# Kernel tuning notes

Measured on AMD Instinct MI355X. Metric: run time of the kernel, lower is better.

The kernel has to match this reference:

```python
import jax, jax.numpy as jnp
import numpy as np
from jax import lax

D_MODEL = 1024
D_INNER = 2 * D_MODEL          # expand=2
D_STATE = 16
D_CONV = 4
DT_RANK = 64                   # ceil(1024/16)
DT_MIN = 0.001
DT_MAX = 0.1
BATCH = 4
SEQ = 2048


def setup_inputs() -> dict:
    key = jax.random.key(0)
    ks = jax.random.split(key, 8)
    s = lambda fan_in: 1.0 / np.sqrt(fan_in)
    x = jax.random.normal(ks[0], (BATCH, SEQ, D_MODEL), dtype=jnp.float32)
    # Linear weights stored as (in, out) so y = x @ W
    W_in = jax.random.uniform(ks[1], (D_MODEL, 2 * D_INNER), jnp.float32, -s(D_MODEL), s(D_MODEL))
    conv_w = jax.random.uniform(ks[2], (D_INNER, 1, D_CONV), jnp.float32, -s(D_CONV), s(D_CONV))
    conv_b = jax.random.uniform(ks[3], (D_INNER,), jnp.float32, -s(D_CONV), s(D_CONV))
    W_x = jax.random.uniform(ks[4], (D_INNER, DT_RANK + 2 * D_STATE), jnp.float32, -s(D_INNER), s(D_INNER))
    W_dt = jax.random.uniform(ks[5], (DT_RANK, D_INNER), jnp.float32, -s(DT_RANK), s(DT_RANK))
    b_dt = jax.random.uniform(ks[6], (D_INNER,), jnp.float32, -s(DT_RANK), s(DT_RANK))
    # A = arange(1..d_state) repeated over d_inner; store log(A)
    A_log = jnp.log(jnp.broadcast_to(jnp.arange(1, D_STATE + 1, dtype=jnp.float32), (D_INNER, D_STATE)))
    D_param = jnp.ones((D_INNER,), dtype=jnp.float32)
    W_out = jax.random.uniform(ks[7], (D_INNER, D_MODEL), jnp.float32, -s(D_INNER), s(D_INNER))
    return {"x": x, "W_in": W_in, "conv_w": conv_w, "conv_b": conv_b,
            "W_x": W_x, "W_dt": W_dt, "b_dt": b_dt, "A_log": A_log,
            "D_param": D_param, "W_out": W_out}


def reference(x, W_in, conv_w, conv_b, W_x, W_dt, b_dt, A_log, D_param, W_out):
    # in_proj + split
    xz = x @ W_in                                   # (B, S, 2*d_inner)
    x_branch, z_branch = jnp.split(xz, 2, axis=-1)  # each (B, S, d_inner)

    # causal depthwise conv1d (torch pads d_conv-1 both sides then slices [:seq])
    xc = jnp.pad(x_branch.transpose(0, 2, 1), ((0, 0), (0, 0), (D_CONV - 1, 0)))
    xc = lax.conv_general_dilated(xc, conv_w, (1,), 'VALID',
                                  dimension_numbers=('NCH', 'OIH', 'NCH'),
                                  feature_group_count=D_INNER)
    xc = xc + conv_b[None, :, None]
    x_conv = jax.nn.silu(xc.transpose(0, 2, 1))     # (B, S, d_inner)

    # input-dependent dt, B, C
    x_dbl = x_conv @ W_x                            # (B, S, dt_rank + 2*d_state)
    dt_low = x_dbl[..., :DT_RANK]
    Bm = x_dbl[..., DT_RANK:DT_RANK + D_STATE]      # (B, S, d_state)
    Cm = x_dbl[..., DT_RANK + D_STATE:]             # (B, S, d_state)
    dt = jax.nn.sigmoid(dt_low @ W_dt + b_dt) * (DT_MAX - DT_MIN) + DT_MIN
    dt = jnp.maximum(dt, 1e-4)                      # (B, S, d_inner)

    A = -jnp.exp(A_log)                             # (d_inner, d_state)

    # selective scan over time (n_substeps = 1)
    def step(h, inp):
        dt_t, B_t, C_t, x_t = inp                   # (B,di), (B,ds), (B,ds), (B,di)
        dA = jnp.exp(dt_t[:, :, None] * A[None])    # (B, di, ds)
        h = dA * h + (dt_t * x_t)[:, :, None] * B_t[:, None, :]
        y_t = jnp.sum(h * C_t[:, None, :], axis=-1) # (B, di)
        return h, y_t

    h0 = jnp.zeros((x.shape[0], D_INNER, D_STATE), dtype=x.dtype)
    _, ys = lax.scan(step, h0,
                     (dt.swapaxes(0, 1), Bm.swapaxes(0, 1),
                      Cm.swapaxes(0, 1), x_conv.swapaxes(0, 1)))
    y = ys.swapaxes(0, 1)                           # (B, S, d_inner)

    y = y + x_conv * D_param
    y = y * jax.nn.silu(z_branch)
    return y @ W_out                                # (B, S, d_model)
```

## Files before the change

kernel.cpp:

```cpp
#include <hip/hip_runtime.h>

typedef unsigned short u16;
typedef unsigned int u32;
typedef __attribute__((ext_vector_type(8))) short short8;
typedef __attribute__((ext_vector_type(4))) short short4v;
typedef __attribute__((ext_vector_type(2))) short short2v;
typedef __attribute__((ext_vector_type(4))) float f32x4;

#define NBATCH 4
#define NSEQ   2048
#define DMODEL 1024
#define DINNER 2048
#define DSTATE 16
#define DTRANK 64
#define ROWS   (NBATCH*NSEQ)
#define NCH    64
#define CLEN   32

__device__ __forceinline__ float b2f(u16 u){ union{u32 i; float f;} v; v.i=((u32)u)<<16; return v.f; }
__device__ __forceinline__ u16 f2b(float f){ union{float f; u32 i;} v; v.f=f; u32 i=v.i; return (u16)((i + 0x7FFFu + ((i>>16)&1u))>>16); }
__device__ __forceinline__ float sigmoidf_(float x){ return 1.0f/(1.0f+__expf(-x)); }

__global__ __launch_bounds__(256) void prep(const u16* __restrict__ x,
    const u16* __restrict__ Win, const u16* __restrict__ convw,
    const u16* __restrict__ Wx, const u16* __restrict__ Wdt,
    const u16* __restrict__ Alog, const u16* __restrict__ Wout,
    const u16* __restrict__ v0, const u16* __restrict__ v1, const u16* __restrict__ v2,
    int* __restrict__ meta){
  __shared__ int vote;
  __shared__ int mxbits;
  const int tid = threadIdx.x;
  const u16* V[3] = {v0, v1, v2};

  const u16* ptrs[6] = {x, Win, convw, Wx, Wdt, Wout};
  const float bounds[6] = {8.f, 0.045f, 0.6f, 0.035f, 0.15f, 0.035f};
  const int slots[6] = {0, 1, 2, 4, 5, 9};
  for (int q = 0; q < 6; q++){
    if (tid == 0) vote = 1;
    __syncthreads();
    int bad = 0;
    for (int i = tid; i < 2048; i += 256){
      float v = fabsf(b2f(ptrs[q][i]));
      if (!(v <= bounds[q])) bad = 1;
    }
    if (bad) atomicAnd(&vote, 0);
    __syncthreads();
    if (tid == 0) meta[slots[q]] = vote;
    __syncthreads();
  }
  if (tid == 0){ u16 u = Alog[1]; meta[7] = (u == 0x3F31 || u == 0x3F32) ? 1 : 0; }

  int iD = -1, fD = 1;
  for (int k = 0; k < 3; k++){
    if (V[k][0] == 0x3F80 && V[k][1] == 0x3F80){ iD = k; fD = 1; }
    else if (V[k][0] == 0 && V[k][1] == 0x3F80 && V[k][2] == 0){ iD = k; fD = 0; }
  }
  if (iD < 0){ iD = 2; fD = 1; }
  int oo[2], no = 0;
  for (int k = 0; k < 3; k++) if (k != iD) oo[no++] = k;
  int fo[2]; float mo[2];
  for (int q = 0; q < 2; q++){
    if (tid == 0) vote = 1;
    __syncthreads();
    int bad = 0;
    for (int i = tid; i < 2048; i += 256){
      float v = fabsf(b2f(V[oo[q]][i]));
      if (!(v <= 0.6f)) bad = 1;
    }
    if (bad) atomicAnd(&vote, 0);
    __syncthreads();
    fo[q] = vote;
    if (tid == 0) mxbits = 0;
    __syncthreads();
    float m = 0.f;
    for (int i = tid; i < 2048; i += 256){
      float v = fabsf(fo[q] ? b2f(V[oo[q]][i]) : ((const float*)V[oo[q]])[i]);
      m = fmaxf(m, v);
    }
    atomicMax(&mxbits, __float_as_int(m));
    __syncthreads();
    mo[q] = __int_as_float(mxbits);
    __syncthreads();
  }
  if (tid == 0){
    int a = (mo[0] > 0.25f) ? 0 : 1;
    meta[10] = oo[a];     meta[3] = fo[a];
    meta[11] = oo[1-a];   meta[6] = fo[1-a];
    meta[12] = iD;        meta[8] = fD;
  }
}

__global__ __launch_bounds__(256) void cvt_bf16(const void* __restrict__ in,
                                                u16* __restrict__ out, long n,
                                                const int* __restrict__ meta, int slot){
  long i = (long)blockIdx.x*256 + threadIdx.x;
  if (i >= n) return;
  if (meta[slot]) out[i] = ((const u16*)in)[i];
  else            out[i] = f2b(((const float*)in)[i]);
}

__global__ __launch_bounds__(256) void cvt_x8(const void* __restrict__ in,
                                              u16* __restrict__ out,
                                              const int* __restrict__ meta){
  long i8 = ((long)blockIdx.x*256 + threadIdx.x)*8;
  if (meta[0]){
    *(short8*)(out + i8) = *(const short8*)((const u16*)in + i8);
  } else {
    const float* f = (const float*)in + i8;
    f32x4 a = *(const f32x4*)f;
    f32x4 b = *(const f32x4*)(f+4);
    short8 o;
    #pragma unroll
    for (int j=0;j<4;j++){ ((u16*)&o)[j] = f2b(a[j]); ((u16*)&o)[4+j] = f2b(b[j]); }
    *(short8*)(out + i8) = o;
  }
}

__global__ __launch_bounds__(256) void cvt_trio(const void* __restrict__ v0,
                                                const void* __restrict__ v1,
                                                const void* __restrict__ v2,
                                                const int* __restrict__ meta,
                                                u16* __restrict__ cbc,
                                                u16* __restrict__ bdtc,
                                                u16* __restrict__ dpc){
  int i = blockIdx.x*256 + threadIdx.x;
  int which = i >> 11, d = i & 2047;
  const void* V[3] = {v0, v1, v2};
  int src, fl; u16* dst;
  if (which == 0){ src = meta[10]; fl = meta[3]; dst = cbc; }
  else if (which == 1){ src = meta[11]; fl = meta[6]; dst = bdtc; }
  else { src = meta[12]; fl = meta[8]; dst = dpc; }
  dst[d] = fl ? ((const u16*)V[src])[d] : f2b(((const float*)V[src])[d]);
}

__global__ __launch_bounds__(256) void transpose_pad(const void* __restrict__ inv,
                                                     u16* __restrict__ out,
                                                     int K, int N, int Nout,
                                                     const int* __restrict__ meta, int slot){
  __shared__ u16 t[32][33];
  const int f = meta[slot];
  const u16*   ib = (const u16*)inv;
  const float* iff = (const float*)inv;
  int k0 = blockIdx.x*32, n0 = blockIdx.y*32;
  int tx = threadIdx.x & 31, ty = threadIdx.x >> 5;
  #pragma unroll
  for (int i=0;i<32;i+=8){
    int k = k0+ty+i, n = n0+tx;
    u16 v = 0;
    if (k<K && n<N) v = f ? ib[(long)k*N+n] : f2b(iff[(long)k*N+n]);
    t[ty+i][tx] = v;
  }
  __syncthreads();
  #pragma unroll
  for (int i=0;i<32;i+=8){
    int n = n0+ty+i, k = k0+tx;
    if (n<Nout && k<K) out[(long)n*K+k] = t[tx][ty+i];
  }
}

template<int MODE>
__global__ __launch_bounds__(256) void gemm_bt(
    const u16* __restrict__ A, int lda,
    const u16* __restrict__ Bt, int K,
    u16* __restrict__ C0, u16* __restrict__ C1, int ldc,
    const u16* __restrict__ bias, float* __restrict__ Cf)
{
  __shared__ u16 sa[128*64];
  __shared__ u16 sb[128*64];
  const int tid = threadIdx.x;
  const int lane = tid & 63;
  const int wave = tid >> 6;
  const int wm = (wave >> 1) * 64;
  const int wn = (wave & 1) * 64;
  const int lane15 = lane & 15;
  const int quad = lane >> 4;
  const long rowBase = (long)blockIdx.y * 128;
  const long colBase = (long)blockIdx.x * 128;

  int kbeg = 0, kend = K;
  if (MODE == 4){
    const int span = K >> 2;
    kbeg = blockIdx.z * span;
    kend = kbeg + span;
    Cf += (long)blockIdx.z * (8192L*128);
  }

  f32x4 acc[4][4];
  #pragma unroll
  for (int i=0;i<4;i++)
    #pragma unroll
    for (int j=0;j<4;j++)
      #pragma unroll
      for (int r=0;r<4;r++) acc[i][j][r]=0.0f;

  const int e  = tid*8;
  const int r0 = e >> 6;
  const int c0 = e & 63;

  for (int kb=kbeg; kb<kend; kb+=64) {
    #pragma unroll
    for (int i=0;i<4;i++){
      const u16* ga = A + (rowBase + r0 + i*32)*lda + kb + c0;
      __builtin_amdgcn_global_load_lds((const __attribute__((address_space(1))) void*)ga,
                                       (__attribute__((address_space(3))) void*)&sa[e + i*2048],
                                       16, 0, 0);
    }
    #pragma unroll
    for (int i=0;i<4;i++){
      const u16* gb = Bt + (colBase + r0 + i*32)*(long)K + kb + c0;
      __builtin_amdgcn_global_load_lds((const __attribute__((address_space(1))) void*)gb,
                                       (__attribute__((address_space(3))) void*)&sb[e + i*2048],
                                       16, 0, 0);
    }
    __syncthreads();
    #pragma unroll
    for (int ko=0; ko<2; ko++){
      const int kk = ko*32 + quad*8;
      short8 af[4], bfr[4];
      #pragma unroll
      for (int i=0;i<4;i++) af[i]  = *(const short8*)&sa[(wm + i*16 + lane15)*64 + kk];
      #pragma unroll
      for (int j=0;j<4;j++) bfr[j] = *(const short8*)&sb[(wn + j*16 + lane15)*64 + kk];
      #pragma unroll
      for (int i=0;i<4;i++)
        #pragma unroll
        for (int j=0;j<4;j++)
          acc[i][j] = __builtin_amdgcn_mfma_f32_16x16x32_bf16(af[i], bfr[j], acc[i][j], 0, 0, 0);
    }
    __syncthreads();
  }

  #pragma unroll
  for (int i=0;i<4;i++){
    #pragma unroll
    for (int j=0;j<4;j++){
      long row = rowBase + wm + i*16 + quad*4;
      long col = colBase + wn + j*16 + lane15;
      #pragma unroll
      for (int r=0;r<4;r++){
        float v = acc[i][j][r];
        long rr = row + r;
        if (MODE == 0) {
          C0[rr*ldc + col] = f2b(v);
        } else if (MODE == 2) {
          float t  = sigmoidf_(v + b2f(bias[col]));
          float dv = fmaxf(t*0.099f + 0.001f, 1e-4f);
          C0[rr*ldc + col] = f2b(dv);
        } else if (MODE == 3 || MODE == 4) {
          Cf[rr*ldc + col] = v;
        }
      }
    }
  }
}

__global__ __launch_bounds__(256) void reduce_xdbl(const float* __restrict__ P,
                                                   u16* __restrict__ out){
  const long i4 = ((long)blockIdx.x*256 + threadIdx.x)*4;
  f32x4 a = *(const f32x4*)(P + i4);
  f32x4 b = *(const f32x4*)(P + 1048576 + i4);
  f32x4 c = *(const f32x4*)(P + 2097152 + i4);
  f32x4 d = *(const f32x4*)(P + 3145728 + i4);
  short4v o;
  #pragma unroll
  for (int j=0;j<4;j++) ((u16*)&o)[j] = f2b(a[j]+b[j]+c[j]+d[j]);
  *(short4v*)(out + i4) = o;
}

template<int IB, int JB>
__device__ __forceinline__ void mm16(f32x4 (&acc)[8][4],
                                     const short8 (&Av)[4][2], const short8 (&Bv)[2][2]){
  #pragma unroll
  for (int s=0;s<2;s++)
    #pragma unroll
    for (int i=0;i<4;i++)
      #pragma unroll
      for (int j=0;j<2;j++)
        acc[IB+i][JB+j] = __builtin_amdgcn_mfma_f32_16x16x32_bf16(Av[i][s], Bv[j][s], acc[IB+i][JB+j], 0, 0, 0);
}

__device__ __forceinline__ void lda4(short8 (&dst)[4][2], const u16* s, int base, int k0, int k1){
  #pragma unroll
  for (int i=0;i<4;i++){
    dst[i][0] = *(const short8*)&s[base + i*1024 + k0];
    dst[i][1] = *(const short8*)&s[base + i*1024 + k1];
  }
}
__device__ __forceinline__ void ldb2(short8 (&dst)[2][2], const u16* s, int base, int k0, int k1){
  #pragma unroll
  for (int j=0;j<2;j++){
    dst[j][0] = *(const short8*)&s[base + j*1024 + k0];
    dst[j][1] = *(const short8*)&s[base + j*1024 + k1];
  }
}

#define GB_SYNC_IN()  do{ asm volatile("s_barrier" ::: "memory"); \
                          asm volatile("s_waitcnt lgkmcnt(0)" ::: "memory"); \
                          __builtin_amdgcn_sched_barrier(0); \
                          __builtin_amdgcn_s_setprio(1); }while(0)
#define GB_SYNC_OUT() do{ __builtin_amdgcn_s_setprio(0); \
                          asm volatile("s_barrier" ::: "memory"); }while(0)
#define GB_SYNC_OUT_VM() do{ __builtin_amdgcn_s_setprio(0); \
                          asm volatile("s_waitcnt vmcnt(6)" ::: "memory"); \
                          asm volatile("s_barrier" ::: "memory"); }while(0)

template<int MODE>
__global__ __launch_bounds__(512, 2) void gemm256(
    const u16* __restrict__ A, int lda,
    const u16* __restrict__ Bt, int K,
    u16* __restrict__ C0, u16* __restrict__ C1, int ldc,
    float* __restrict__ Cf)
{
  __shared__ u16 sa[2*16384];
  __shared__ u16 sb[2*16384];
  const int tid  = threadIdx.x;
  const int lane = tid & 63;
  const int wm   = (tid >> 6) >> 2;
  const int wn   = (tid >> 6) & 3;
  const int lane15 = lane & 15;
  const int quad   = lane >> 4;

  const int nwg  = gridDim.x * gridDim.y;
  const int orig = blockIdx.y * gridDim.x + blockIdx.x;
  const int swz  = (orig & 7) * (nwg >> 3) + (orig >> 3);
  const int bx   = swz % gridDim.x;
  const int by   = swz / gridDim.x;
  const long rowBase = (long)by * 256;
  const long colBase = (long)bx * 256;

  const int xorv = (lane15 & 7) << 3;
  const int k0   = (quad*8) ^ xorv;
  const int k1   = (32 + quad*8) ^ xorv;
  const int aBase = (wm*128 + lane15) * 64;
  const int bBase = (wn*64  + lane15) * 64;

  const int scol = ((tid & 7) ^ ((tid >> 3) & 7)) << 3;
  const int arow = tid >> 3;
  const int bsub = ((tid >> 8) & 1)*64 + ((tid & 255) >> 3);
  const int bdst = (tid & 7) * 8;

  f32x4 acc[8][4];
  #pragma unroll
  for (int i=0;i<8;i++)
    #pragma unroll
    for (int j=0;j<4;j++)
      #pragma unroll
      for (int r=0;r<4;r++) acc[i][j][r]=0.0f;

  const int nt = K >> 6;

  auto stageA = [&](int buf, int rs, int kb){
    const u16* g = A + (rowBase + rs + arow)*(long)lda + kb + scol;
    __builtin_amdgcn_global_load_lds((const __attribute__((address_space(1))) void*)g,
        (__attribute__((address_space(3))) void*)&sa[buf*16384 + rs*64 + tid*8], 16, 0, 0);
  };
  auto stageB = [&](int buf, int cq, int part, int kb){
    const int row = part*128 + cq*32 + bsub;
    const u16* g = Bt + (colBase + row)*(long)K + kb + scol;
    __builtin_amdgcn_global_load_lds((const __attribute__((address_space(1))) void*)g,
        (__attribute__((address_space(3))) void*)&sb[buf*16384 + row*64 + bdst], 16, 0, 0);
  };
  auto stageAh = [&](int buf, int h, int kb){ stageA(buf, h*64, kb); stageA(buf, 128 + h*64, kb); };
  auto stageBc = [&](int buf, int cq, int kb){ stageB(buf, cq, 0, kb); stageB(buf, cq, 1, kb); };

  stageAh(0,0,0);  stageBc(0,0,0);  stageAh(0,1,0);  stageBc(0,1,0);
  stageAh(1,0,64); stageBc(1,0,64); stageAh(1,1,64);
  asm volatile("s_waitcnt vmcnt(6)" ::: "memory");
  asm volatile("s_barrier" ::: "memory");

  const u16* sA0 = &sa[0];      const u16* sB0 = &sb[0];
  const u16* sA1 = &sa[16384];  const u16* sB1 = &sb[16384];
  short8 a0[4][2], a1[4][2], b0[2][2], b1[2][2];

  for (int it = 0; it < (nt >> 1); ++it){
    const int kb = it << 7;

    lda4(a0, sA0, aBase, k0, k1);
    ldb2(b0, sB0, bBase, k0, k1);
    stageBc(1, 1, kb + 64);
    GB_SYNC_IN();  mm16<0,0>(acc, a0, b0);  GB_SYNC_OUT();
    lda4(a1, sA0, aBase + 4096, k0, k1);
    stageAh(0, 0, kb + 128);
    GB_SYNC_IN();  mm16<4,0>(acc, a1, b0);  GB_SYNC_OUT();
    ldb2(b1, sB0, bBase + 2048, k0, k1);
    stageBc(0, 0, kb + 128);
    GB_SYNC_IN();  mm16<0,2>(acc, a0, b1);  GB_SYNC_OUT();
    stageAh(0, 1, kb + 128);
    GB_SYNC_IN();  mm16<4,2>(acc, a1, b1);  GB_SYNC_OUT_VM();

    lda4(a0, sA1, aBase, k0, k1);
    ldb2(b0, sB1, bBase, k0, k1);
    stageBc(0, 1, kb + 128);
    GB_SYNC_IN();  mm16<0,0>(acc, a0, b0);  GB_SYNC_OUT();
    lda4(a1, sA1, aBase + 4096, k0, k1);
    stageAh(1, 0, kb + 192);
    GB_SYNC_IN();  mm16<4,0>(acc, a1, b0);  GB_SYNC_OUT();
    ldb2(b1, sB1, bBase + 2048, k0, k1);
    stageBc(1, 0, kb + 192);
    GB_SYNC_IN();  mm16<0,2>(acc, a0, b1);  GB_SYNC_OUT();
    stageAh(1, 1, kb + 192);
    GB_SYNC_IN();  mm16<4,2>(acc, a1, b1);  GB_SYNC_OUT_VM();
  }

  #pragma unroll
  for (int i=0;i<8;i++){
    const long row = rowBase + wm*128 + i*16 + quad*4;
    #pragma unroll
    for (int j=0;j<4;j++){
      const long col = colBase + wn*64 + j*16 + lane15;
      #pragma unroll
      for (int r=0;r<4;r++){
        const float v = acc[i][j][r];
        const long rr = row + r;
        if (MODE == 1){
          if (col < 2048) C0[rr*2048 + col] = f2b(v);
          else            C1[rr*2048 + (col-2048)] = f2b(v);
        } else {
          Cf[rr*ldc + col] = v;
        }
      }
    }
  }
}

__global__ __launch_bounds__(256) void conv_silu(const u16* __restrict__ xb,
                                                 const u16* __restrict__ w,
                                                 const u16* __restrict__ bias,
                                                 u16* __restrict__ xc){
  long idx8 = ((long)blockIdx.x*256 + threadIdx.x) * 8;
  int d = (int)(idx8 & (DINNER-1));
  int s = (int)((idx8 >> 11) & (NSEQ-1));
  int b = (int)(idx8 >> 22);

  short8 bv = *(const short8*)(bias + d);
  short8 wv0 = *(const short8*)(w + d*4);
  short8 wv1 = *(const short8*)(w + d*4 + 8);
  short8 wv2 = *(const short8*)(w + d*4 + 16);
  short8 wv3 = *(const short8*)(w + d*4 + 24);
  u16 wl[32];
  #pragma unroll
  for (int q=0;q<8;q++){ wl[q] = ((u16*)&wv0)[q]; wl[8+q] = ((u16*)&wv1)[q];
                         wl[16+q] = ((u16*)&wv2)[q]; wl[24+q] = ((u16*)&wv3)[q]; }

  float acc[8];
  #pragma unroll
  for (int l=0;l<8;l++) acc[l] = b2f(((u16*)&bv)[l]);

  #pragma unroll
  for (int j=0;j<4;j++){
    int t = s - 3 + j;
    if (t >= 0){
      short8 xv = *(const short8*)(xb + ((long)(b*NSEQ + t))*DINNER + d);
      #pragma unroll
      for (int l=0;l<8;l++)
        acc[l] += b2f(((u16*)&xv)[l]) * b2f(wl[l*4 + j]);
    }
  }
  short8 ov;
  #pragma unroll
  for (int l=0;l<8;l++){ float y = acc[l]*sigmoidf_(acc[l]); ((u16*)&ov)[l] = f2b(y); }
  *(short8*)(xc + idx8) = ov;
}

__global__ __launch_bounds__(256) void scan_pass1(const u16* __restrict__ dt,
                                                  const u16* __restrict__ xc,
                                                  const u16* __restrict__ xdbl,
                                                  const u16* __restrict__ Alog,
                                                  float* __restrict__ hend,
                                                  float* __restrict__ sumdt){
  const int tid = threadIdx.x;
  const int d0 = blockIdx.x*512 + tid*2;
  const int c = blockIdx.y;
  const int b = blockIdx.z;
  __shared__ float sB[CLEN][DSTATE];
  for (int i=tid; i<CLEN*DSTATE; i+=256){
    int t = i >> 4, s = i & 15;
    sB[t][s] = b2f(xdbl[((long)(b*NSEQ + c*CLEN + t))*128 + DTRANK + s]);
  }
  bool fast = true;
  #pragma unroll
  for (int j=0;j<2;j++)
    #pragma unroll
    for (int s=0;s<DSTATE;s++){
      float a = -__expf(b2f(Alog[(d0+j)*DSTATE + s]));
      fast = fast && (fabsf(a + (float)(s+1)) < 0.03f*(float)(s+1));
    }
  __syncthreads();

  float h[2][DSTATE];
  #pragma unroll
  for (int j=0;j<2;j++)
    #pragma unroll
    for (int s=0;s<DSTATE;s++) h[j][s] = 0.0f;
  float sd[2] = {0.f,0.f};
  long base = ((long)(b*NSEQ + c*CLEN))*DINNER + d0;
  short2v dt2 = *(const short2v*)(dt + base);
  short2v x2  = *(const short2v*)(xc + base);
  if (fast){
    for (int t=0;t<CLEN;t++){
      long nxt = base + (long)((t+1<CLEN)?(t+1):t)*DINNER;
      short2v dtn = *(const short2v*)(dt + nxt);
      short2v xn  = *(const short2v*)(xc + nxt);
      float B[DSTATE];
      *(f32x4*)&B[0]  = *(const f32x4*)&sB[t][0];
      *(f32x4*)&B[4]  = *(const f32x4*)&sB[t][4];
      *(f32x4*)&B[8]  = *(const f32x4*)&sB[t][8];
      *(f32x4*)&B[12] = *(const f32x4*)&sB[t][12];
      #pragma unroll
      for (int j=0;j<2;j++){
        float dtv = b2f(((u16*)&dt2)[j]);
        float xv  = b2f(((u16*)&x2)[j]);
        float u = dtv*xv;
        sd[j] += dtv;
        float e1 = __expf(-dtv);
        float p = e1;
        #pragma unroll
        for (int s=0;s<DSTATE;s++){
          h[j][s] = fmaf(p, h[j][s], u*B[s]);
          p *= e1;
        }
      }
      dt2 = dtn; x2 = xn;
    }
  } else {
    float Acf[2][DSTATE];
    #pragma unroll
    for (int j=0;j<2;j++)
      #pragma unroll
      for (int s=0;s<DSTATE;s++) Acf[j][s] = -__expf(b2f(Alog[(d0+j)*DSTATE + s]));
    for (int t=0;t<CLEN;t++){
      long nxt = base + (long)((t+1<CLEN)?(t+1):t)*DINNER;
      short2v dtn = *(const short2v*)(dt + nxt);
      short2v xn  = *(const short2v*)(xc + nxt);
      float B[DSTATE];
      *(f32x4*)&B[0]  = *(const f32x4*)&sB[t][0];
      *(f32x4*)&B[4]  = *(const f32x4*)&sB[t][4];
      *(f32x4*)&B[8]  = *(const f32x4*)&sB[t][8];
      *(f32x4*)&B[12] = *(const f32x4*)&sB[t][12];
      #pragma unroll
      for (int j=0;j<2;j++){
        float dtv = b2f(((u16*)&dt2)[j]);
        float xv  = b2f(((u16*)&x2)[j]);
        float u = dtv*xv;
        sd[j] += dtv;
        #pragma unroll
        for (int s=0;s<DSTATE;s++){
          float dA = __expf(dtv * Acf[j][s]);
          h[j][s] = fmaf(dA, h[j][s], u*B[s]);
        }
      }
      dt2 = dtn; x2 = xn;
    }
  }
  #pragma unroll
  for (int j=0;j<2;j++){
    long hidx = ((long)(b*DINNER + d0 + j)*NCH + c)*DSTATE;
    #pragma unroll
    for (int q=0;q<4;q++) *(f32x4*)&hend[hidx + q*4] = *(const f32x4*)&h[j][q*4];
    sumdt[(long)(b*DINNER + d0 + j)*NCH + c] = sd[j];
  }
}

__global__ __launch_bounds__(256) void scan_pass2(float* __restrict__ hend,
                                                  const float* __restrict__ sumdt,
                                                  const u16* __restrict__ Alog){
  long i = (long)blockIdx.x*256 + threadIdx.x;
  int s = (int)(i & 15);
  long bd = i >> 4;
  int d = (int)(bd & (DINNER-1));
  float A = -__expf(b2f(Alog[d*DSTATE + s]));
  float run = 0.0f;
  long base = bd*NCH*DSTATE + s;
  for (int c=0;c<NCH;c++){
    float e = hend[base + (long)c*DSTATE];
    float decay = __expf(A * sumdt[bd*NCH + c]);
    hend[base + (long)c*DSTATE] = run;
    run = run*decay + e;
  }
}

__global__ __launch_bounds__(256) void scan_pass3(const u16* __restrict__ dt,
                                                  u16* __restrict__ xc,
                                                  const u16* __restrict__ zb,
                                                  const u16* __restrict__ xdbl,
                                                  const u16* __restrict__ Alog,
                                                  const u16* __restrict__ Dp,
                                                  const float* __restrict__ hstart){
  const int tid = threadIdx.x;
  const int d0 = blockIdx.x*512 + tid*2;
  const int c = blockIdx.y;
  const int b = blockIdx.z;
  __shared__ float sB[CLEN][DSTATE];
  __shared__ float sC[CLEN][DSTATE];
  for (int i=tid; i<CLEN*DSTATE; i+=256){
    int t = i >> 4, s = i & 15;
    long rb = ((long)(b*NSEQ + c*CLEN + t))*128;
    sB[t][s] = b2f(xdbl[rb + DTRANK + s]);
    sC[t][s] = b2f(xdbl[rb + DTRANK + DSTATE + s]);
  }
  bool fast = true;
  #pragma unroll
  for (int j=0;j<2;j++)
    #pragma unroll
    for (int s=0;s<DSTATE;s++){
      float a = -__expf(b2f(Alog[(d0+j)*DSTATE + s]));
      fast = fast && (fabsf(a + (float)(s+1)) < 0.03f*(float)(s+1));
    }
  __syncthreads();

  float h[2][DSTATE];
  #pragma unroll
  for (int j=0;j<2;j++){
    long hidx = ((long)(b*DINNER + d0 + j)*NCH + c)*DSTATE;
    #pragma unroll
    for (int q=0;q<4;q++) *(f32x4*)&h[j][q*4] = *(const f32x4*)&hstart[hidx + q*4];
  }
  short2v dp2 = *(const short2v*)(Dp + d0);
  long base = ((long)(b*NSEQ + c*CLEN))*DINNER + d0;
  short2v dt2 = *(const short2v*)(dt + base);
  short2v x2  = *(const short2v*)(xc + base);
  short2v z2  = *(const short2v*)(zb + base);
  if (fast){
    for (int t=0;t<CLEN;t++){
      long nxt = base + (long)((t+1<CLEN)?(t+1):t)*DINNER;
      short2v dtn = *(const short2v*)(dt + nxt);
      short2v xn  = *(const short2v*)(xc + nxt);
      short2v zn  = *(const short2v*)(zb + nxt);
      float B[DSTATE], C[DSTATE];
      *(f32x4*)&B[0]  = *(const f32x4*)&sB[t][0];
      *(f32x4*)&B[4]  = *(const f32x4*)&sB[t][4];
      *(f32x4*)&B[8]  = *(const f32x4*)&sB[t][8];
      *(f32x4*)&B[12] = *(const f32x4*)&sB[t][12];
      *(f32x4*)&C[0]  = *(const f32x4*)&sC[t][0];
      *(f32x4*)&C[4]  = *(const f32x4*)&sC[t][4];
      *(f32x4*)&C[8]  = *(const f32x4*)&sC[t][8];
      *(f32x4*)&C[12] = *(const f32x4*)&sC[t][12];
      short2v ov;
      #pragma unroll
      for (int j=0;j<2;j++){
        float dtv = b2f(((u16*)&dt2)[j]);
        float xv  = b2f(((u16*)&x2)[j]);
        float zv  = b2f(((u16*)&z2)[j]);
        float u = dtv*xv;
        float e1 = __expf(-dtv);
        float gate = zv*sigmoidf_(zv);
        float p = e1;
        float y = 0.0f;
        #pragma unroll
        for (int s=0;s<DSTATE;s++){
          h[j][s] = fmaf(p, h[j][s], u*B[s]);
          y = fmaf(h[j][s], C[s], y);
          p *= e1;
        }
        y = fmaf(xv, b2f(((u16*)&dp2)[j]), y);
        y *= gate;
        ((u16*)&ov)[j] = f2b(y);
      }
      *(short2v*)(xc + base + (long)t*DINNER) = ov;
      dt2 = dtn; x2 = xn; z2 = zn;
    }
  } else {
    float Acf[2][DSTATE];
    #pragma unroll
    for (int j=0;j<2;j++)
      #pragma unroll
      for (int s=0;s<DSTATE;s++) Acf[j][s] = -__expf(b2f(Alog[(d0+j)*DSTATE + s]));
    for (int t=0;t<CLEN;t++){
      long nxt = base + (long)((t+1<CLEN)?(t+1):t)*DINNER;
      short2v dtn = *(const short2v*)(dt + nxt);
      short2v xn  = *(const short2v*)(xc + nxt);
      short2v zn  = *(const short2v*)(zb + nxt);
      float B[DSTATE], C[DSTATE];
      *(f32x4*)&B[0]  = *(const f32x4*)&sB[t][0];
      *(f32x4*)&B[4]  = *(const f32x4*)&sB[t][4];
      *(f32x4*)&B[8]  = *(const f32x4*)&sB[t][8];
      *(f32x4*)&B[12] = *(const f32x4*)&sB[t][12];
      *(f32x4*)&C[0]  = *(const f32x4*)&sC[t][0];
      *(f32x4*)&C[4]  = *(const f32x4*)&sC[t][4];
      *(f32x4*)&C[8]  = *(const f32x4*)&sC[t][8];
      *(f32x4*)&C[12] = *(const f32x4*)&sC[t][12];
      short2v ov;
      #pragma unroll
      for (int j=0;j<2;j++){
        float dtv = b2f(((u16*)&dt2)[j]);
        float xv  = b2f(((u16*)&x2)[j]);
        float zv  = b2f(((u16*)&z2)[j]);
        float u = dtv*xv;
        float gate = zv*sigmoidf_(zv);
        float y = 0.0f;
        #pragma unroll
        for (int s=0;s<DSTATE;s++){
          float dA = __expf(dtv * Acf[j][s]);
          h[j][s] = fmaf(dA, h[j][s], u*B[s]);
          y = fmaf(h[j][s], C[s], y);
        }
        y = fmaf(xv, b2f(((u16*)&dp2)[j]), y);
        y *= gate;
        ((u16*)&ov)[j] = f2b(y);
      }
      *(short2v*)(xc + base + (long)t*DINNER) = ov;
      dt2 = dtn; x2 = xn; z2 = zn;
    }
  }
}

extern "C" void kernel_launch(void* const* d_in, const int* in_sizes, int n_in,
                              void* d_out, int out_size, void* d_ws, size_t ws_size,
                              hipStream_t stream) {
  const void *x=nullptr,*W_in=nullptr,*conv_w=nullptr,*W_x=nullptr,*W_dt=nullptr,
             *A_log=nullptr,*W_out=nullptr;
  const void* v2048[3] = {nullptr,nullptr,nullptr};
  int n2048 = 0;
  for (int i = 0; i < n_in; i++){
    switch (in_sizes[i]){
      case 8388608: x      = d_in[i]; break;
      case 4194304: W_in   = d_in[i]; break;
      case 8192:    conv_w = d_in[i]; break;
      case 196608:  W_x    = d_in[i]; break;
      case 131072:  W_dt   = d_in[i]; break;
      case 32768:   A_log  = d_in[i]; break;
      case 2097152: W_out  = d_in[i]; break;
      case 2048:    if (n2048 < 3) v2048[n2048++] = d_in[i]; break;
      default: break;
    }
  }

  size_t off = 0;
  char* wsb = (char*)d_ws;
  auto take = [&](size_t n){ void* p = wsb + off; off += (n + 255) & ~(size_t)255; return p; };
  u16* Wt_in  = (u16*)take((size_t)4096*1024*2);
  u16* Wt_x   = (u16*)take((size_t)128*2048*2);
  u16* Wt_dt  = (u16*)take((size_t)2048*64*2);
  u16* Wt_out = (u16*)take((size_t)1024*2048*2);
  u16* xb     = (u16*)take((size_t)ROWS*DINNER*2);
  u16* zb     = (u16*)take((size_t)ROWS*DINNER*2);
  u16* xc     = (u16*)take((size_t)ROWS*DINNER*2);
  u16* xdbl   = (u16*)take((size_t)ROWS*128*2);
  char* shr = (char*)take((size_t)ROWS*NCH*DSTATE*4 + (size_t)ROWS*NCH*4 + 4096);
  u16*   xcvt  = (u16*)shr;
  float* hend  = (float*)shr;
  float* sumdt = (float*)(shr + (size_t)ROWS*NCH*DSTATE*4);
  u16* cwc  = (u16*)take(DINNER*4*2);
  u16* cbc  = (u16*)take(DINNER*2);
  u16* bdtc = (u16*)take(DINNER*2);
  u16* alc  = (u16*)take(DINNER*DSTATE*2);
  u16* dpc  = (u16*)take(DINNER*2);
  int* meta = (int*)take(256);
  float* xdp = (float*)take((size_t)4*8192*128*4);
  u16* dtb = xb;

  prep<<<1, 256, 0, stream>>>((const u16*)x, (const u16*)W_in, (const u16*)conv_w,
                              (const u16*)W_x, (const u16*)W_dt, (const u16*)A_log,
                              (const u16*)W_out,
                              (const u16*)v2048[0], (const u16*)v2048[1], (const u16*)v2048[2],
                              meta);

  cvt_x8<<<(ROWS*DMODEL)/(256*8), 256, 0, stream>>>(x, xcvt, meta);
  cvt_bf16<<<32, 256, 0, stream>>>(conv_w, cwc, DINNER*4, meta, 2);
  cvt_bf16<<<128,256, 0, stream>>>(A_log, alc, DINNER*DSTATE, meta, 7);
  cvt_trio<<<24, 256, 0, stream>>>(v2048[0], v2048[1], v2048[2], meta, cbc, bdtc, dpc);

  transpose_pad<<<dim3(32,128), 256, 0, stream>>>(W_in, Wt_in, 1024, 4096, 4096, meta, 1);
  transpose_pad<<<dim3(64,4),   256, 0, stream>>>(W_x,  Wt_x,  2048, 96,   128,  meta, 4);
  transpose_pad<<<dim3(2,64),   256, 0, stream>>>(W_dt, Wt_dt, 64,   2048, 2048, meta, 5);
  transpose_pad<<<dim3(64,32),  256, 0, stream>>>(W_out,Wt_out,2048, 1024, 1024, meta, 9);

  gemm256<1><<<dim3(16,32), 512, 0, stream>>>(xcvt, 1024, Wt_in, 1024, xb, zb, 2048, nullptr);

  conv_silu<<<(ROWS*DINNER)/(256*8), 256, 0, stream>>>(xb, cwc, cbc, xc);

  gemm_bt<4><<<dim3(1,64,4), 256, 0, stream>>>(xc, 2048, Wt_x, 2048, nullptr, nullptr, 128, nullptr, xdp);
  reduce_xdbl<<<1024, 256, 0, stream>>>(xdp, xdbl);

  gemm_bt<2><<<dim3(16,64), 256, 0, stream>>>(xdbl, 128, Wt_dt, 64, dtb, nullptr, 2048, bdtc, nullptr);

  scan_pass1<<<dim3(4,NCH,NBATCH), 256, 0, stream>>>(dtb, xc, xdbl, alc, hend, sumdt);
  scan_pass2<<<(ROWS*DSTATE)/256, 256, 0, stream>>>(hend, sumdt, alc);
  scan_pass3<<<dim3(4,NCH,NBATCH), 256, 0, stream>>>(dtb, xc, zb, xdbl, alc, dpc, hend);

  gemm_bt<3><<<dim3(8,64), 256, 0, stream>>>(xc, 2048, Wt_out, 2048, nullptr, nullptr, 1024, nullptr, (float*)d_out);
}
```

Before: 485.5 us.

## Restructure GEMM main loop to single-step double buffering; shorten scan dependency chains

Replaces the two-step unrolled GEMM pipeline, with its per-phase double barriers and helper macros, by a per-K-tile loop. Each loop iteration prefetches the next tile into the alternate buffer in quarters, interleaved with the four MFMA quadrants, and uses fewer barriers with vmcnt(4) waits. In the selective scan fast paths, the serial power chain p*=e1 is replaced by a log-depth computation of e1^1..e1^16. The y reduction is split into four independent accumulators to shorten dependency chains. The GEMM change alters prefetch distance and synchronisation, which risks less memory-latency hiding.

```diff
diff --git a/kernel.cpp b/kernel.cpp
--- a/kernel.cpp
+++ b/kernel.cpp
@@ -20,6 +20,14 @@
 __device__ __forceinline__ float b2f(u16 u){ union{u32 i; float f;} v; v.i=((u32)u)<<16; return v.f; }
 __device__ __forceinline__ u16 f2b(float f){ union{float f; u32 i;} v; v.f=f; u32 i=v.i; return (u16)((i + 0x7FFFu + ((i>>16)&1u))>>16); }
 __device__ __forceinline__ float sigmoidf_(float x){ return 1.0f/(1.0f+__expf(-x)); }
+
+__device__ __forceinline__ void pow16(float e1, float (&pw)[16]){
+  float p2 = e1*e1, p4 = p2*p2, p8 = p4*p4;
+  pw[0]=e1;        pw[1]=p2;        pw[2]=e1*p2;     pw[3]=p4;
+  pw[4]=e1*p4;     pw[5]=p2*p4;     pw[6]=pw[2]*p4;  pw[7]=p8;
+  pw[8]=e1*p8;     pw[9]=p2*p8;     pw[10]=pw[2]*p8; pw[11]=p4*p8;
+  pw[12]=pw[4]*p8; pw[13]=pw[5]*p8; pw[14]=pw[6]*p8; pw[15]=p8*p8;
+}
 
 __global__ __launch_bounds__(256) void prep(const u16* __restrict__ x,
     const u16* __restrict__ Win, const u16* __restrict__ convw,
@@ -267,43 +275,6 @@
   *(short4v*)(out + i4) = o;
 }
 
-template<int IB, int JB>
-__device__ __forceinline__ void mm16(f32x4 (&acc)[8][4],
-                                     const short8 (&Av)[4][2], const short8 (&Bv)[2][2]){
-  #pragma unroll
-  for (int s=0;s<2;s++)
-    #pragma unroll
-    for (int i=0;i<4;i++)
-      #pragma unroll
-      for (int j=0;j<2;j++)
-        acc[IB+i][JB+j] = __builtin_amdgcn_mfma_f32_16x16x32_bf16(Av[i][s], Bv[j][s], acc[IB+i][JB+j], 0, 0, 0);
-}
-
-__device__ __forceinline__ void lda4(short8 (&dst)[4][2], const u16* s, int base, int k0, int k1){
-  #pragma unroll
-  for (int i=0;i<4;i++){
-    dst[i][0] = *(const short8*)&s[base + i*1024 + k0];
-    dst[i][1] = *(const short8*)&s[base + i*1024 + k1];
-  }
-}
-__device__ __forceinline__ void ldb2(short8 (&dst)[2][2], const u16* s, int base, int k0, int k1){
-  #pragma unroll
-  for (int j=0;j<2;j++){
-    dst[j][0] = *(const short8*)&s[base + j*1024 + k0];
-    dst[j][1] = *(const short8*)&s[base + j*1024 + k1];
-  }
-}
-
-#define GB_SYNC_IN()  do{ asm volatile("s_barrier" ::: "memory"); \
-                          asm volatile("s_waitcnt lgkmcnt(0)" ::: "memory"); \
-                          __builtin_amdgcn_sched_barrier(0); \
-                          __builtin_amdgcn_s_setprio(1); }while(0)
-#define GB_SYNC_OUT() do{ __builtin_amdgcn_s_setprio(0); \
-                          asm volatile("s_barrier" ::: "memory"); }while(0)
-#define GB_SYNC_OUT_VM() do{ __builtin_amdgcn_s_setprio(0); \
-                          asm volatile("s_waitcnt vmcnt(6)" ::: "memory"); \
-                          asm volatile("s_barrier" ::: "memory"); }while(0)
-
 template<int MODE>
 __global__ __launch_bounds__(512, 2) void gemm256(
     const u16* __restrict__ A, int lda,
@@ -360,46 +331,88 @@
     __builtin_amdgcn_global_load_lds((const __attribute__((address_space(1))) void*)g,
         (__attribute__((address_space(3))) void*)&sb[buf*16384 + row*64 + bdst], 16, 0, 0);
   };
-  auto stageAh = [&](int buf, int h, int kb){ stageA(buf, h*64, kb); stageA(buf, 128 + h*64, kb); };
-  auto stageBc = [&](int buf, int cq, int kb){ stageB(buf, cq, 0, kb); stageB(buf, cq, 1, kb); };
-
-  stageAh(0,0,0);  stageBc(0,0,0);  stageAh(0,1,0);  stageBc(0,1,0);
-  stageAh(1,0,64); stageBc(1,0,64); stageAh(1,1,64);
-  asm volatile("s_waitcnt vmcnt(6)" ::: "memory");
-  asm volatile("s_barrier" ::: "memory");
-
-  const u16* sA0 = &sa[0];      const u16* sB0 = &sb[0];
-  const u16* sA1 = &sa[16384];  const u16* sB1 = &sb[16384];
-  short8 a0[4][2], a1[4][2], b0[2][2], b1[2][2];
-
-  for (int it = 0; it < (nt >> 1); ++it){
-    const int kb = it << 7;
-
-    lda4(a0, sA0, aBase, k0, k1);
-    ldb2(b0, sB0, bBase, k0, k1);
-    stageBc(1, 1, kb + 64);
-    GB_SYNC_IN();  mm16<0,0>(acc, a0, b0);  GB_SYNC_OUT();
-    lda4(a1, sA0, aBase + 4096, k0, k1);
-    stageAh(0, 0, kb + 128);
-    GB_SYNC_IN();  mm16<4,0>(acc, a1, b0);  GB_SYNC_OUT();
-    ldb2(b1, sB0, bBase + 2048, k0, k1);
-    stageBc(0, 0, kb + 128);
-    GB_SYNC_IN();  mm16<0,2>(acc, a0, b1);  GB_SYNC_OUT();
-    stageAh(0, 1, kb + 128);
-    GB_SYNC_IN();  mm16<4,2>(acc, a1, b1);  GB_SYNC_OUT_VM();
-
-    lda4(a0, sA1, aBase, k0, k1);
-    ldb2(b0, sB1, bBase, k0, k1);
-    stageBc(0, 1, kb + 128);
-    GB_SYNC_IN();  mm16<0,0>(acc, a0, b0);  GB_SYNC_OUT();
-    lda4(a1, sA1, aBase + 4096, k0, k1);
-    stageAh(1, 0, kb + 192);
-    GB_SYNC_IN();  mm16<4,0>(acc, a1, b0);  GB_SYNC_OUT();
-    ldb2(b1, sB1, bBase + 2048, k0, k1);
-    stageBc(1, 0, kb + 192);
-    GB_SYNC_IN();  mm16<0,2>(acc, a0, b1);  GB_SYNC_OUT();
-    stageAh(1, 1, kb + 192);
-    GB_SYNC_IN();  mm16<4,2>(acc, a1, b1);  GB_SYNC_OUT_VM();
+
+  stageA(0,   0, 0); stageA(0, 128, 0);
+  stageB(0, 0, 0, 0); stageB(0, 0, 1, 0);
+  stageA(0,  64, 0); stageA(0, 192, 0);
+  stageB(0, 1, 0, 0); stageB(0, 1, 1, 0);
+  asm volatile("s_waitcnt vmcnt(4)\n\ts_barrier" ::: "memory");
+
+  for (int t = 0; t < nt; ++t){
+    const int cur = t & 1, nb = cur ^ 1;
+    const int kb2 = (t+1) << 6;
+    const bool pf = (t+1 < nt);
+    const u16* sA = &sa[cur*16384];
+    const u16* sB = &sb[cur*16384];
+    short8 a0[4][2], a1[4][2], b0[2][2], b1[2][2];
+
+    #pragma unroll
+    for (int i=0;i<4;i++){
+      a0[i][0] = *(const short8*)&sA[aBase + i*1024 + k0];
+      a0[i][1] = *(const short8*)&sA[aBase + i*1024 + k1];
+    }
+    #pragma unroll
+    for (int j=0;j<2;j++){
+      b0[j][0] = *(const short8*)&sB[bBase + j*1024 + k0];
+      b0[j][1] = *(const short8*)&sB[bBase + j*1024 + k1];
+    }
+    if (pf){ stageA(nb, 0, kb2); stageA(nb, 128, kb2); }
+    __builtin_amdgcn_s_setprio(1);
+    #pragma unroll
+    for (int s=0;s<2;s++)
+      #pragma unroll
+      for (int i=0;i<4;i++)
+        #pragma unroll
+        for (int j=0;j<2;j++)
+          acc[i][j] = __builtin_amdgcn_mfma_f32_16x16x32_bf16(a0[i][s], b0[j][s], acc[i][j], 0, 0, 0);
+    __builtin_amdgcn_s_setprio(0);
+    asm volatile("s_waitcnt vmcnt(4)\n\ts_barrier" ::: "memory");
+
+    #pragma unroll
+    for (int i=0;i<4;i++){
+      a1[i][0] = *(const short8*)&sA[aBase + 4096 + i*1024 + k0];
+      a1[i][1] = *(const short8*)&sA[aBase + 4096 + i*1024 + k1];
+    }
+    if (pf){ stageB(nb, 0, 0, kb2); stageB(nb, 0, 1, kb2); }
+    __builtin_amdgcn_s_setprio(1);
+    #pragma unroll
+    for (int s=0;s<2;s++)
+      #pragma unroll
+      for (int i=0;i<4;i++)
+        #pragma unroll
+        for (int j=0;j<2;j++)
+          acc[4+i][j] = __builtin_amdgcn_mfma_f32_16x16x32_bf16(a1[i][s], b0[j][s], acc[4+i][j], 0, 0, 0);
+    __builtin_amdgcn_s_setprio(0);
+    asm volatile("s_waitcnt vmcnt(4)\n\ts_barrier" ::: "memory");
+
+    #pragma unroll
+    for (int j=0;j<2;j++){
+      b1[j][0] = *(const short8*)&sB[bBase + 2048 + j*1024 + k0];
+      b1[j][1] = *(const short8*)&sB[bBase + 2048 + j*1024 + k1];
+    }
+    if (pf){ stageA(nb, 64, kb2); stageA(nb, 192, kb2); }
+    __builtin_amdgcn_s_setprio(1);
+    #pragma unroll
+    for (int s=0;s<2;s++)
+      #pragma unroll
+      for (int i=0;i<4;i++)
+        #pragma unroll
+        for (int j=0;j<2;j++)
+          acc[i][2+j] = __builtin_amdgcn_mfma_f32_16x16x32_bf16(a0[i][s], b1[j][s], acc[i][2+j], 0, 0, 0);
+    __builtin_amdgcn_s_setprio(0);
+    asm volatile("s_barrier" ::: "memory");
+
+    if (pf){ stageB(nb, 1, 0, kb2); stageB(nb, 1, 1, kb2); }
+    __builtin_amdgcn_s_setprio(1);
+    #pragma unroll
+    for (int s=0;s<2;s++)
+      #pragma unroll
+      for (int i=0;i<4;i++)
+        #pragma unroll
+        for (int j=0;j<2;j++)
+          acc[4+i][2+j] = __builtin_amdgcn_mfma_f32_16x16x32_bf16(a1[i][s], b1[j][s], acc[4+i][2+j], 0, 0, 0);
+    __builtin_amdgcn_s_setprio(0);
+    asm volatile("s_waitcnt vmcnt(4)\n\ts_barrier" ::: "memory");
   }
 
   #pragma unroll
@@ -513,12 +526,11 @@
         float u = dtv*xv;
         sd[j] += dtv;
         float e1 = __expf(-dtv);
-        float p = e1;
+        float pw[16];
+        pow16(e1, pw);
         #pragma unroll
-        for (int s=0;s<DSTATE;s++){
-          h[j][s] = fmaf(p, h[j][s], u*B[s]);
-          p *= e1;
-        }
+        for (int s=0;s<DSTATE;s++)
+          h[j][s] = fmaf(pw[s], h[j][s], u*B[s]);
       }
       dt2 = dtn; x2 = xn;
     }
@@ -644,14 +656,21 @@
         float u = dtv*xv;
         float e1 = __expf(-dtv);
         float gate = zv*sigmoidf_(zv);
-        float p = e1;
-        float y = 0.0f;
+        float pw[16];
+        pow16(e1, pw);
+        float y0=0.f, y1=0.f, y2=0.f, y3=0.f;
         #pragma unroll
-        for (int s=0;s<DSTATE;s++){
-          h[j][s] = fmaf(p, h[j][s], u*B[s]);
-          y = fmaf(h[j][s], C[s], y);
-          p *= e1;
+        for (int q=0;q<4;q++){
+          h[j][q*4+0] = fmaf(pw[q*4+0], h[j][q*4+0], u*B[q*4+0]);
+          h[j][q*4+1] = fmaf(pw[q*4+1], h[j][q*4+1], u*B[q*4+1]);
+          h[j][q*4+2] = fmaf(pw[q*4+2], h[j][q*4+2], u*B[q*4+2]);
+          h[j][q*4+3] = fmaf(pw[q*4+3], h[j][q*4+3], u*B[q*4+3]);
+          y0 = fmaf(h[j][q*4+0], C[q*4+0], y0);
+          y1 = fmaf(h[j][q*4+1], C[q*4+1], y1);
+          y2 = fmaf(h[j][q*4+2], C[q*4+2], y2);
+          y3 = fmaf(h[j][q*4+3], C[q*4+3], y3);
         }
+        float y = (y0+y1)+(y2+y3);
         y = fmaf(xv, b2f(((u16*)&dp2)[j]), y);
         y *= gate;
         ((u16*)&ov)[j] = f2b(y);
```

New measurement: 466.8 us. 1.04x faster.
